# Performance work log

Measured on AMD Instinct MI355X. Metric: run time of the kernel, lower is better.

Reference implementation:

```python
import jax, jax.numpy as jnp
import numpy as np
import math

B, LL, LP = 16, 256, 1024
HID, H = 128, 8
SCALE = math.sqrt(HID)


def setup_inputs() -> dict:
    key = jax.random.key(0)
    ks = jax.random.split(key, 20)
    s = 0.02
    inp = {
        "ligand": jax.random.normal(ks[0], (B, LL, HID), jnp.float32),
        "prot": jax.random.normal(ks[1], (B, LP, HID), jnp.float32),
        "inter": jax.random.uniform(ks[2], (B, 1, LL, LP), jnp.float32),
        # projection weights stored as [in, out] (x @ W + b)
        "Wl1": jax.random.normal(ks[3], (HID, HID * H), jnp.float32) * s,
        "bl1": jnp.zeros((HID * H,), jnp.float32),
        "Wl2": jax.random.normal(ks[4], (HID, HID * H), jnp.float32) * s,
        "bl2": jnp.zeros((HID * H,), jnp.float32),
        "Wp1": jax.random.normal(ks[5], (HID, HID * H), jnp.float32) * s,
        "bp1": jnp.zeros((HID * H,), jnp.float32),
        "Wp2": jax.random.normal(ks[6], (HID, HID * H), jnp.float32) * s,
        "bp2": jnp.zeros((HID * H,), jnp.float32),
        "W11": jax.random.normal(ks[7], (HID * H, HID), jnp.float32) * s,
        "b11": jnp.zeros((HID,), jnp.float32),
        "W12": jax.random.normal(ks[8], (2 * HID, HID), jnp.float32) * s,
        "b12": jnp.zeros((HID,), jnp.float32),
        "W21": jax.random.normal(ks[9], (HID * H, HID), jnp.float32) * s,
        "b21": jnp.zeros((HID,), jnp.float32),
        "W22": jax.random.normal(ks[10], (2 * HID, HID), jnp.float32) * s,
        "b22": jnp.zeros((HID,), jnp.float32),
    }
    return inp


def _heads(x):
    # [B, L, H*D] -> [B, H, L, D]
    b, l, _ = x.shape
    return x.reshape(b, l, H, HID).transpose(0, 2, 1, 3)


def reference(ligand, prot, inter, Wl1, bl1, Wl2, bl2, Wp1, bp1, Wp2, bp2,
              W11, b11, W12, b12, W21, b21, W22, b22):
    relu = jax.nn.relu
    l1 = _heads(relu(ligand @ Wl1 + bl1))   # [B,H,LL,D]
    l2 = _heads(relu(ligand @ Wl2 + bl2))   # [B,H,LL,D]
    p1 = _heads(relu(prot @ Wp1 + bp1))     # [B,H,LP,D]
    p2 = _heads(relu(prot @ Wp2 + bp2))     # [B,H,LP,D]

    energy = jnp.einsum('bhld,bhpd->bhlp', l1, p1) / SCALE
    att = jax.nn.softmax(energy * inter, axis=-1)  # dropout is identity at eval

    # ligand branch: att @ prot2 -> [B,LL,H*D]
    lig3 = jnp.einsum('bhlp,bhpd->blhd', att, p2).reshape(B, LL, H * HID)
    lig3 = jnp.concatenate([lig3 @ W11 + b11, ligand], axis=2)
    lig3 = relu(lig3 @ W12 + b12)

    # protein branch: att^T @ ligand2 -> [B,LP,H*D]
    prot3 = jnp.einsum('bhlp,bhld->bphd', att, l2).reshape(B, LP, H * HID)
    prot3 = jnp.concatenate([prot3 @ W21 + b21, prot], axis=2)
    prot3 = relu(prot3 @ W22 + b22)
    return (lig3, prot3)
```

## Files before the change

kernel.cpp:

```cpp
#include <hip/hip_runtime.h>
#include <hip/hip_bf16.h>

typedef unsigned short u16;
typedef __attribute__((ext_vector_type(4))) float f32x4;
typedef __attribute__((ext_vector_type(4))) unsigned int u32x4;
typedef __attribute__((ext_vector_type(4))) unsigned short u16x4;
typedef __attribute__((ext_vector_type(8))) unsigned short u16x8;
typedef __attribute__((ext_vector_type(8))) __bf16 bf16x8;

__device__ inline float u2f(u16 u) {
    union { unsigned int i; float f; } x; x.i = ((unsigned int)u) << 16; return x.f;
}
__device__ inline u16 f2u(float f) {
    __hip_bfloat16 b = __float2bfloat16(f);
    return *reinterpret_cast<u16*>(&b);
}
__device__ inline f32x4 mfma16(bf16x8 a, bf16x8 b, f32x4 c) {
    return __builtin_amdgcn_mfma_f32_16x16x32_bf16(a, b, c, 0, 0, 0);
}
__device__ inline void gload_lds16(const u16* g, u16* l) {
    __builtin_amdgcn_global_load_lds(
        (const __attribute__((address_space(1))) unsigned int*)g,
        (__attribute__((address_space(3))) unsigned int*)l, 16, 0, 0);
}

__global__ __launch_bounds__(256)
void proj_kernel(const u16* __restrict__ ligb, const u16* __restrict__ protb,
                 const u16* __restrict__ Wl1t, const u16* __restrict__ Wl2t,
                 const u16* __restrict__ Wp1t, const u16* __restrict__ Wp2t,
                 const float* __restrict__ bl1, const float* __restrict__ bl2,
                 const float* __restrict__ bp1, const float* __restrict__ bp2,
                 u16* __restrict__ l1v, u16* __restrict__ l2tv,
                 u16* __restrict__ p1v, u16* __restrict__ p2tv)
{
    __shared__ __align__(16) u16 As[128 * 64];
    __shared__ __align__(16) u16 Bs[128 * 64];
    const int y = blockIdx.y;
    const u16* A; const u16* B; const float* bias; u16* Out;
    int mode, logL, my;
    if (y < 32)       { A = ligb;  B = Wl1t; bias = bl1; Out = l1v;  mode = 1; logL = 8;  my = y; }
    else if (y < 64)  { A = ligb;  B = Wl2t; bias = bl2; Out = l2tv; mode = 3; logL = 8;  my = y - 32; }
    else if (y < 192) { A = protb; B = Wp1t; bias = bp1; Out = p1v;  mode = 1; logL = 10; my = y - 64; }
    else              { A = protb; B = Wp2t; bias = bp2; Out = p2tv; mode = 3; logL = 10; my = y - 192; }
    const int n0 = blockIdx.x * 128, m0 = my * 128;
    const int tid = threadIdx.x;
    const int w = tid >> 6, lane = tid & 63, q = lane >> 4, li = lane & 15;
    const int wr = w >> 1, wc = w & 1;

    const int srow = tid >> 3;
    const int cg = (tid & 7) ^ (srow & 7);
    const int ldsbase = ((tid >> 6) * 8) * 64;

    f32x4 acc[4][4];
    #pragma unroll
    for (int i = 0; i < 4; i++)
        #pragma unroll
        for (int j = 0; j < 4; j++) acc[i][j] = (f32x4){0.f, 0.f, 0.f, 0.f};

    #pragma unroll
    for (int kt = 0; kt < 128; kt += 64) {
        const u16* Ab = A + (long)m0 * 128 + kt + cg * 8;
        const u16* Bb = B + (long)n0 * 128 + kt + cg * 8;
        #pragma unroll
        for (int c = 0; c < 4; c++) {
            gload_lds16(Ab + (long)(c * 32 + srow) * 128, &As[ldsbase + c * 32 * 64]);
            gload_lds16(Bb + (long)(c * 32 + srow) * 128, &Bs[ldsbase + c * 32 * 64]);
        }
        __syncthreads();
        #pragma unroll
        for (int s = 0; s < 2; s++) {
            const int cp = ((s * 4 + q) ^ (li & 7)) * 8;
            bf16x8 av[4], bv[4];
            #pragma unroll
            for (int i = 0; i < 4; i++)
                av[i] = *(bf16x8*)&As[(wr * 64 + i * 16 + li) * 64 + cp];
            #pragma unroll
            for (int j = 0; j < 4; j++)
                bv[j] = *(bf16x8*)&Bs[(wc * 64 + j * 16 + li) * 64 + cp];
            #pragma unroll
            for (int i = 0; i < 4; i++)
                #pragma unroll
                for (int j = 0; j < 4; j++)
                    acc[i][j] = mfma16(av[i], bv[j], acc[i][j]);
        }
        __syncthreads();
    }

    const int Lm = (1 << logL) - 1;
    #pragma unroll
    for (int i = 0; i < 4; i++) {
        #pragma unroll
        for (int j = 0; j < 4; j++) {
            const int col = n0 + wc * 64 + j * 16 + li;
            const float bvs = bias[col];
            if (mode == 3) {
                const int row0 = m0 + wr * 64 + i * 16 + q * 4;
                long base = ((long)(((row0 >> logL) * 8 + (col >> 7)) * 128
                            + (col & 127)) << logL) + (row0 & Lm);
                u16x4 o;
                #pragma unroll
                for (int r = 0; r < 4; r++)
                    o[r] = f2u(fmaxf(acc[i][j][r] + bvs, 0.f));
                *(u16x4*)(Out + base) = o;
            } else {
                #pragma unroll
                for (int r = 0; r < 4; r++) {
                    const int row = m0 + wr * 64 + i * 16 + q * 4 + r;
                    long addr = ((long)((row >> logL) * 8 + (col >> 7)) << (logL + 7))
                              + ((long)(row & Lm) << 7) + (col & 127);
                    Out[addr] = f2u(fmaxf(acc[i][j][r] + bvs, 0.f));
                }
            }
        }
    }
}

__global__ __launch_bounds__(512)
void av_kernel(const u16* __restrict__ att, const u16* __restrict__ p2t,
               const u16* __restrict__ l2t,
               u16* __restrict__ lig3, u16* __restrict__ prot3)
{
    __shared__ __align__(16) u16 As[256 * 64];
    __shared__ __align__(16) u16 Bs[128 * 64];
    __shared__ __align__(16) u16 T[64 * 256];
    const int bid = blockIdx.x;
    const int tid = threadIdx.x;
    const int w = tid >> 6, lane = tid & 63, q = lane >> 4, li = lane & 15;
    const int wr = w >> 1, wc = w & 1;

    f32x4 acc[4][4];
    #pragma unroll
    for (int i = 0; i < 4; i++)
        #pragma unroll
        for (int j = 0; j < 4; j++) acc[i][j] = (f32x4){0.f, 0.f, 0.f, 0.f};

    if (bid < 128) {
        const int bh = bid;
        const u16* A = att + (long)bh * 262144;
        const u16* B = p2t + (long)bh * 131072;
        const int srow = tid >> 3;
        const int cg = (tid & 7) ^ (srow & 7);
        const int ldsbase = ((tid >> 6) * 8) * 64;

        for (int kt = 0; kt < 1024; kt += 64) {
            const u16* Ab = A + kt + cg * 8;
            const u16* Bb = B + kt + cg * 8;
            #pragma unroll
            for (int c = 0; c < 4; c++)
                gload_lds16(Ab + (long)(c * 64 + srow) * 1024,
                            &As[ldsbase + c * 64 * 64]);
            #pragma unroll
            for (int c = 0; c < 2; c++)
                gload_lds16(Bb + (long)(c * 64 + srow) * 1024,
                            &Bs[ldsbase + c * 64 * 64]);
            __syncthreads();
            #pragma unroll
            for (int s = 0; s < 2; s++) {
                const int cp = ((s * 4 + q) ^ (li & 7)) * 8;
                bf16x8 av[4], bv[4];
                #pragma unroll
                for (int i = 0; i < 4; i++)
                    av[i] = *(bf16x8*)&As[(wr * 64 + i * 16 + li) * 64 + cp];
                #pragma unroll
                for (int j = 0; j < 4; j++)
                    bv[j] = *(bf16x8*)&Bs[(wc * 64 + j * 16 + li) * 64 + cp];
                #pragma unroll
                for (int i = 0; i < 4; i++)
                    #pragma unroll
                    for (int j = 0; j < 4; j++)
                        acc[i][j] = mfma16(av[i], bv[j], acc[i][j]);
            }
            __syncthreads();
        }

        const long obase = ((long)(bh >> 3) * 256) * 1024 + (long)(bh & 7) * 128;
        #pragma unroll
        for (int i = 0; i < 4; i++)
            #pragma unroll
            for (int j = 0; j < 4; j++) {
                const int col = wc * 64 + j * 16 + li;
                #pragma unroll
                for (int r = 0; r < 4; r++) {
                    const int row = wr * 64 + i * 16 + q * 4 + r;
                    lig3[obase + (long)row * 1024 + col] = f2u(acc[i][j][r]);
                }
            }
    } else {
        const int pb = bid - 128;
        const int bh = pb >> 2;
        const int m0 = (pb & 3) * 256;
        const u16* A = att + (long)bh * 262144;
        const u16* B = l2t + (long)bh * 32768;
        const int w6 = tid >> 6;
        const int i5 = (tid >> 5) & 1;
        const int srow = tid >> 3;
        const int cg = (tid & 7) ^ (srow & 7);
        const int bldsbase = w6 * 8 * 64;

        for (int kt = 0; kt < 256; kt += 64) {
            #pragma unroll
            for (int c = 0; c < 4; c++) {
                gload_lds16(A + (long)(kt + w6 * 8 + c * 2 + i5) * 1024
                              + m0 + (tid & 31) * 8,
                            &T[w6 * 2048 + c * 512]);
            }
            #pragma unroll
            for (int c = 0; c < 2; c++)
                gload_lds16(B + (long)(c * 64 + srow) * 256 + kt + cg * 8,
                            &Bs[bldsbase + c * 64 * 64]);
            __syncthreads();

            #pragma unroll
            for (int pass = 0; pass < 4; pass++) {
                const int p = pass * 64 + (tid & 63);
                union { u16 e[8]; u32x4 v; } tmp;
                #pragma unroll
                for (int e = 0; e < 8; e++)
                    tmp.e[e] = T[(w6 * 8 + e) * 256 + p];
                *(u32x4*)&As[p * 64 + ((w6 ^ (p & 7)) * 8)] = tmp.v;
            }
            __syncthreads();

            #pragma unroll
            for (int s = 0; s < 2; s++) {
                const int cp = ((s * 4 + q) ^ (li & 7)) * 8;
                bf16x8 av[4], bv[4];
                #pragma unroll
                for (int i = 0; i < 4; i++)
                    av[i] = *(bf16x8*)&As[(wr * 64 + i * 16 + li) * 64 + cp];
                #pragma unroll
                for (int j = 0; j < 4; j++)
                    bv[j] = *(bf16x8*)&Bs[(wc * 64 + j * 16 + li) * 64 + cp];
                #pragma unroll
                for (int i = 0; i < 4; i++)
                    #pragma unroll
                    for (int j = 0; j < 4; j++)
                        acc[i][j] = mfma16(av[i], bv[j], acc[i][j]);
            }
            __syncthreads();
        }

        const long obase = ((long)(bh >> 3) * 1024 + m0) * 1024 + (long)(bh & 7) * 128;
        #pragma unroll
        for (int i = 0; i < 4; i++)
            #pragma unroll
            for (int j = 0; j < 4; j++) {
                const int col = wc * 64 + j * 16 + li;
                #pragma unroll
                for (int r = 0; r < 4; r++) {
                    const int row = wr * 64 + i * 16 + q * 4 + r;
                    prot3[obase + (long)row * 1024 + col] = f2u(acc[i][j][r]);
                }
            }
    }
}

__global__ __launch_bounds__(256)
void finals_kernel(const u16* __restrict__ lig3, const u16* __restrict__ ligb,
                   const u16* __restrict__ WstL, const float* __restrict__ bcL,
                   float* __restrict__ out0,
                   const u16* __restrict__ prot3, const u16* __restrict__ protb,
                   const u16* __restrict__ WstP, const float* __restrict__ bcP,
                   float* __restrict__ out1)
{
    __shared__ __align__(16) u16 As[128 * 64];
    __shared__ __align__(16) u16 Bs[128 * 64];
    const int y = blockIdx.y;
    const u16 *A, *A2, *B; const float* bias; float* Out; int my;
    if (y < 32) { A = lig3;  A2 = ligb;  B = WstL; bias = bcL; Out = out0; my = y; }
    else        { A = prot3; A2 = protb; B = WstP; bias = bcP; Out = out1; my = y - 32; }
    const int m0 = my * 128;
    const int tid = threadIdx.x;
    const int w = tid >> 6, lane = tid & 63, q = lane >> 4, li = lane & 15;
    const int wr = w >> 1, wc = w & 1;

    const int srow = tid >> 3;
    const int cg = (tid & 7) ^ (srow & 7);
    const int ldsbase = ((tid >> 6) * 8) * 64;

    f32x4 acc[4][4];
    #pragma unroll
    for (int i = 0; i < 4; i++)
        #pragma unroll
        for (int j = 0; j < 4; j++) acc[i][j] = (f32x4){0.f, 0.f, 0.f, 0.f};

    for (int kt = 0; kt < 1152; kt += 64) {
        const u16* Abase; long lda; int ktA;
        if (kt >= 1024) { Abase = A2; lda = 128; ktA = kt - 1024; }
        else            { Abase = A;  lda = 1024; ktA = kt; }
        const u16* Ab = Abase + (long)m0 * lda + ktA + cg * 8;
        const u16* Bb = B + kt + cg * 8;
        #pragma unroll
        for (int c = 0; c < 4; c++) {
            gload_lds16(Ab + (long)(c * 32 + srow) * lda,  &As[ldsbase + c * 32 * 64]);
            gload_lds16(Bb + (long)(c * 32 + srow) * 1152, &Bs[ldsbase + c * 32 * 64]);
        }
        __syncthreads();
        #pragma unroll
        for (int s = 0; s < 2; s++) {
            const int cp = ((s * 4 + q) ^ (li & 7)) * 8;
            bf16x8 av[4], bv[4];
            #pragma unroll
            for (int i = 0; i < 4; i++)
                av[i] = *(bf16x8*)&As[(wr * 64 + i * 16 + li) * 64 + cp];
            #pragma unroll
            for (int j = 0; j < 4; j++)
                bv[j] = *(bf16x8*)&Bs[(wc * 64 + j * 16 + li) * 64 + cp];
            #pragma unroll
            for (int i = 0; i < 4; i++)
                #pragma unroll
                for (int j = 0; j < 4; j++)
                    acc[i][j] = mfma16(av[i], bv[j], acc[i][j]);
        }
        __syncthreads();
    }

    #pragma unroll
    for (int i = 0; i < 4; i++)
        #pragma unroll
        for (int j = 0; j < 4; j++) {
            const int col = wc * 64 + j * 16 + li;
            const float bvs = bias[col];
            #pragma unroll
            for (int r = 0; r < 4; r++) {
                const int row = m0 + wr * 64 + i * 16 + q * 4 + r;
                Out[(long)row * 128 + col] = fmaxf(acc[i][j][r] + bvs, 0.f);
            }
        }
}

__global__ __launch_bounds__(512, 4)
void attn_kernel(const u16* __restrict__ l1, const u16* __restrict__ p1,
                 const u16* __restrict__ interb, u16* __restrict__ att)
{
    __shared__ __align__(16) u16 S[32 * 1024];
    const int id = blockIdx.x;
    const int bh = (id & 7) * 16 + (id >> 6);
    const int mt = (id >> 3) & 7;
    const int b  = bh >> 3;
    const int m0 = mt * 32;
    const int tid = threadIdx.x;
    const float rscale = 0.08838834764831845f;

    {
        const int w = tid >> 6, lane = tid & 63, q = lane >> 4, li = lane & 15;
        bf16x8 af[2][4];
        #pragma unroll
        for (int g = 0; g < 2; g++) {
            const u16* lp = l1 + ((long)bh * 256 + m0 + g * 16 + li) * 128 + q * 8;
            #pragma unroll
            for (int s = 0; s < 4; s++) af[g][s] = *(const bf16x8*)(lp + s * 32);
        }
        const u16* bp0 = p1 + ((long)bh * 1024 + w * 128 + li) * 128 + q * 8;
        #pragma unroll
        for (int pf = 0; pf < 8; pf++) {
            const u16* bp = bp0 + (long)pf * 2048;
            bf16x8 bv[4];
            #pragma unroll
            for (int s = 0; s < 4; s++) bv[s] = *(const bf16x8*)(bp + s * 32);
            f32x4 acc0 = (f32x4){0.f, 0.f, 0.f, 0.f};
            f32x4 acc1 = (f32x4){0.f, 0.f, 0.f, 0.f};
            #pragma unroll
            for (int s = 0; s < 4; s++) {
                acc0 = mfma16(af[0][s], bv[s], acc0);
                acc1 = mfma16(af[1][s], bv[s], acc1);
            }
            const int col = w * 128 + pf * 16 + li;
            #pragma unroll
            for (int r = 0; r < 4; r++) {
                const int row0 = q * 4 + r;
                S[(row0 << 10) + (col ^ ((row0 >> 2) << 4))] = f2u(acc0[r] * rscale);
                const int row1 = 16 + q * 4 + r;
                S[(row1 << 10) + (col ^ ((row1 >> 2) << 4))] = f2u(acc1[r] * rscale);
            }
        }
    }
    __syncthreads();

    const int row = tid >> 4;
    const int lj  = tid & 15;
    const int l   = m0 + row;
    const int sw2 = (row >> 2) << 4;
    const u16* ib = interb + ((long)b * 256 + l) * 1024;

    float mx = -1e30f;
    #pragma unroll
    for (int blk = 0; blk < 8; blk++) {
        const int c = blk * 128 + lj * 8;
        u16* sp = &S[(row << 10) + (c ^ sw2)];
        u16x8 s8 = *(u16x8*)sp;
        u16x8 i8 = *(const u16x8*)(ib + c);
        u16x8 o8;
        #pragma unroll
        for (int e = 0; e < 8; e++) {
            float v = u2f(s8[e]) * u2f(i8[e]);
            mx = fmaxf(mx, v);
            o8[e] = f2u(v);
        }
        *(u16x8*)sp = o8;
    }
    #pragma unroll
    for (int d = 1; d < 16; d <<= 1) mx = fmaxf(mx, __shfl_xor(mx, d, 64));

    float z = 0.f;
    #pragma unroll
    for (int blk = 0; blk < 8; blk++) {
        const int c = blk * 128 + lj * 8;
        u16x8 p8 = *(u16x8*)&S[(row << 10) + (c ^ sw2)];
        #pragma unroll
        for (int e = 0; e < 8; e++) z += __expf(u2f(p8[e]) - mx);
    }
    #pragma unroll
    for (int d = 1; d < 16; d <<= 1) z += __shfl_xor(z, d, 64);
    const float inv = 1.f / z;

    u16* op = att + ((long)bh * 256 + l) * 1024;
    #pragma unroll
    for (int blk = 0; blk < 8; blk++) {
        const int c = blk * 128 + lj * 8;
        u16x8 p8 = *(u16x8*)&S[(row << 10) + (c ^ sw2)];
        u16x8 o8;
        #pragma unroll
        for (int e = 0; e < 8; e++)
            o8[e] = f2u(__expf(u2f(p8[e]) - mx) * inv);
        *(u16x8*)(op + c) = o8;
    }
}

struct TPF { const float* src; u16* dst; int R; int C; };
struct TPF8 { TPF t[8]; };

__global__ __launch_bounds__(256)
void cvtw_kernel(TPF8 args)
{
    TPF tp = args.t[blockIdx.z];
    const int c0 = blockIdx.x * 32, r0 = blockIdx.y * 32;
    if (c0 >= tp.C || r0 >= tp.R) return;
    __shared__ u16 tile[32][33];
    const int tx = threadIdx.x & 31, ty = threadIdx.x >> 5;
    #pragma unroll
    for (int i = 0; i < 4; i++)
        tile[ty + i * 8][tx] = f2u(tp.src[(long)(r0 + ty + i * 8) * tp.C + c0 + tx]);
    __syncthreads();
    #pragma unroll
    for (int i = 0; i < 4; i++)
        tp.dst[(long)(c0 + ty + i * 8) * tp.R + r0 + tx] = tile[tx][ty + i * 8];
}

__global__ __launch_bounds__(256)
void wcomb_kernel(const u16* __restrict__ Wm0, const u16* __restrict__ Wo0,
                  const float* __restrict__ bm0, const float* __restrict__ bo0,
                  u16* __restrict__ Wst0, float* __restrict__ bc0,
                  const u16* __restrict__ Wm1, const u16* __restrict__ Wo1,
                  const float* __restrict__ bm1, const float* __restrict__ bo1,
                  u16* __restrict__ Wst1, float* __restrict__ bc1)
{
    const int zz = blockIdx.y;
    const u16* Wm = zz ? Wm1 : Wm0;
    const u16* Wo = zz ? Wo1 : Wo0;
    const float* bmid = zz ? bm1 : bm0;
    const float* bout = zz ? bo1 : bo0;
    u16* Wst = zz ? Wst1 : Wst0;
    float* bc = zz ? bc1 : bc0;
    const int n = blockIdx.x;
    const int tid = threadIdx.x;
    __shared__ float wrow[128];
    if (tid < 128) wrow[tid] = u2f(Wo[n * 256 + tid]);
    __syncthreads();
    for (int k = tid; k < 1024; k += 256) {
        float acc = 0.f;
        #pragma unroll 4
        for (int j = 0; j < 128; j++) acc += wrow[j] * u2f(Wm[(long)j * 1024 + k]);
        Wst[(long)n * 1152 + k] = f2u(acc);
    }
    if (tid < 128) Wst[(long)n * 1152 + 1024 + tid] = Wo[n * 256 + 128 + tid];
    if (tid == 0) {
        float acc = bout[n];
        for (int j = 0; j < 128; j++) acc += bmid[j] * wrow[j];
        bc[n] = acc;
    }
}

__global__ __launch_bounds__(256)
void cvt3_kernel(const float* __restrict__ a, u16* __restrict__ da, int na,
                 const float* __restrict__ b, u16* __restrict__ db, int nb,
                 const float* __restrict__ c, u16* __restrict__ dc, int nc)
{
    const int zz = blockIdx.y;
    const float* s = zz == 0 ? a : (zz == 1 ? b : c);
    u16* d = zz == 0 ? da : (zz == 1 ? db : dc);
    const int n = zz == 0 ? na : (zz == 1 ? nb : nc);
    const int i = (blockIdx.x * 256 + threadIdx.x) * 4;
    if (i >= n) return;
    const float4 v = *(const float4*)(s + i);
    u16x4 o;
    o.x = f2u(v.x); o.y = f2u(v.y); o.z = f2u(v.z); o.w = f2u(v.w);
    *(u16x4*)(d + i) = o;
}

extern "C" void kernel_launch(void* const* d_in, const int* in_sizes, int n_in,
                              void* d_out, int out_size, void* d_ws, size_t ws_size,
                              hipStream_t stream)
{
    (void)in_sizes; (void)n_in; (void)out_size; (void)ws_size;
    const float* ligand = (const float*)d_in[0];
    const float* prot   = (const float*)d_in[1];
    const float* inter  = (const float*)d_in[2];
    const float* Wl1 = (const float*)d_in[3];  const float* bl1 = (const float*)d_in[4];
    const float* Wl2 = (const float*)d_in[5];  const float* bl2 = (const float*)d_in[6];
    const float* Wp1 = (const float*)d_in[7];  const float* bp1 = (const float*)d_in[8];
    const float* Wp2 = (const float*)d_in[9];  const float* bp2 = (const float*)d_in[10];
    const float* W11 = (const float*)d_in[11]; const float* b11 = (const float*)d_in[12];
    const float* W12 = (const float*)d_in[13]; const float* b12 = (const float*)d_in[14];
    const float* W21 = (const float*)d_in[15]; const float* b21 = (const float*)d_in[16];
    const float* W22 = (const float*)d_in[17]; const float* b22 = (const float*)d_in[18];

    float* out0 = (float*)d_out;
    float* out1 = out0 + (size_t)16 * 256 * 128;

    u16* ws = (u16*)d_ws;
    size_t off = 0;
    auto alloc = [&](size_t n) { u16* p = ws + off; off += n; return p; };
    u16* ligb  = alloc(524288);
    u16* protb = alloc(2097152);
    u16* l1v   = alloc(4194304);
    u16* l2t   = alloc(4194304);
    u16* p1v   = alloc(16777216);
    u16* p2t   = alloc(16777216);
    u16* attv  = alloc(33554432);
    u16* lig3  = alloc(4194304);
    u16* prot3 = alloc(16777216);
    u16* Wl1t  = alloc(131072);
    u16* Wl2t  = alloc(131072);
    u16* Wp1t  = alloc(131072);
    u16* Wp2t  = alloc(131072);
    u16* W11t  = alloc(131072);
    u16* W21t  = alloc(131072);
    u16* W12t  = alloc(32768);
    u16* W22t  = alloc(32768);
    u16* WstL  = alloc(147456);
    u16* WstP  = alloc(147456);
    float* bcL = (float*)alloc(256);
    float* bcP = (float*)alloc(256);

    u16* interb = lig3;

    cvt3_kernel<<<dim3(4096, 3), 256, 0, stream>>>(
        ligand, ligb, 524288, prot, protb, 2097152, inter, interb, 4194304);

    TPF8 tp;
    tp.t[0] = {Wl1, Wl1t, 128, 1024};
    tp.t[1] = {Wl2, Wl2t, 128, 1024};
    tp.t[2] = {Wp1, Wp1t, 128, 1024};
    tp.t[3] = {Wp2, Wp2t, 128, 1024};
    tp.t[4] = {W11, W11t, 1024, 128};
    tp.t[5] = {W21, W21t, 1024, 128};
    tp.t[6] = {W12, W12t, 256, 128};
    tp.t[7] = {W22, W22t, 256, 128};
    cvtw_kernel<<<dim3(32, 32, 8), 256, 0, stream>>>(tp);

    wcomb_kernel<<<dim3(128, 2), 256, 0, stream>>>(
        W11t, W12t, b11, b12, WstL, bcL,
        W21t, W22t, b21, b22, WstP, bcP);

    proj_kernel<<<dim3(8, 320), 256, 0, stream>>>(
        ligb, protb, Wl1t, Wl2t, Wp1t, Wp2t,
        bl1, bl2, bp1, bp2, l1v, l2t, p1v, p2t);

    attn_kernel<<<dim3(1024), 512, 0, stream>>>(l1v, p1v, interb, attv);

    av_kernel<<<dim3(640), 512, 0, stream>>>(attv, p2t, l2t, lig3, prot3);

    finals_kernel<<<dim3(1, 160), 256, 0, stream>>>(
        lig3, ligb, WstL, bcL, out0,
        prot3, protb, WstP, bcP, out1);
}
```

Before: 294.1 us.

## Keep attention scores in registers, remap av blocks, halve finals tile rows

The attention kernel now keeps the QK^T scores in MFMA accumulators, multiplies by the interaction map in registers, and does the softmax max and sum reductions with shuffles plus small cross-wave shared arrays. This removes the 64KB shared score buffer, which should raise occupancy. The AV kernel assigns blocks so that the five blocks for one batch-head run next to each other, aiming for L2 reuse of the attention tile. The finals GEMM tiles drop from 128 to 64 rows, doubling the grid for better CU fill. The trade-offs are scattered 2-byte global loads of the interaction map and stores of the attention output in the MFMA layout instead of 16-byte vectors.

Measured after the change: 311.4 us. +5.9%, slower.

```diff
diff --git a/kernel.cpp b/kernel.cpp
--- a/kernel.cpp
+++ b/kernel.cpp
@@ -123,7 +123,10 @@
     __shared__ __align__(16) u16 As[256 * 64];
     __shared__ __align__(16) u16 Bs[128 * 64];
     __shared__ __align__(16) u16 T[64 * 256];
-    const int bid = blockIdx.x;
+    const int id = blockIdx.x;
+    const int slot = id >> 3;
+    const int bh = (id & 7) * 16 + slot / 5;
+    const int role = slot % 5;
     const int tid = threadIdx.x;
     const int w = tid >> 6, lane = tid & 63, q = lane >> 4, li = lane & 15;
     const int wr = w >> 1, wc = w & 1;
@@ -134,8 +137,7 @@
         #pragma unroll
         for (int j = 0; j < 4; j++) acc[i][j] = (f32x4){0.f, 0.f, 0.f, 0.f};
 
-    if (bid < 128) {
-        const int bh = bid;
+    if (role == 0) {
         const u16* A = att + (long)bh * 262144;
         const u16* B = p2t + (long)bh * 131072;
         const int srow = tid >> 3;
@@ -186,9 +188,7 @@
                 }
             }
     } else {
-        const int pb = bid - 128;
-        const int bh = pb >> 2;
-        const int m0 = (pb & 3) * 256;
+        const int m0 = (role - 1) * 256;
         const u16* A = att + (long)bh * 262144;
         const u16* B = l2t + (long)bh * 32768;
         const int w6 = tid >> 6;
@@ -263,13 +263,13 @@
                    const u16* __restrict__ WstP, const float* __restrict__ bcP,
                    float* __restrict__ out1)
 {
-    __shared__ __align__(16) u16 As[128 * 64];
+    __shared__ __align__(16) u16 As[64 * 64];
     __shared__ __align__(16) u16 Bs[128 * 64];
     const int y = blockIdx.y;
     const u16 *A, *A2, *B; const float* bias; float* Out; int my;
-    if (y < 32) { A = lig3;  A2 = ligb;  B = WstL; bias = bcL; Out = out0; my = y; }
-    else        { A = prot3; A2 = protb; B = WstP; bias = bcP; Out = out1; my = y - 32; }
-    const int m0 = my * 128;
+    if (y < 64) { A = lig3;  A2 = ligb;  B = WstL; bias = bcL; Out = out0; my = y; }
+    else        { A = prot3; A2 = protb; B = WstP; bias = bcP; Out = out1; my = y - 64; }
+    const int m0 = my * 64;
     const int tid = threadIdx.x;
     const int w = tid >> 6, lane = tid & 63, q = lane >> 4, li = lane & 15;
     const int wr = w >> 1, wc = w & 1;
@@ -278,9 +278,9 @@
     const int cg = (tid & 7) ^ (srow & 7);
     const int ldsbase = ((tid >> 6) * 8) * 64;
 
-    f32x4 acc[4][4];
-    #pragma unroll
-    for (int i = 0; i < 4; i++)
+    f32x4 acc[2][4];
+    #pragma unroll
+    for (int i = 0; i < 2; i++)
         #pragma unroll
         for (int j = 0; j < 4; j++) acc[i][j] = (f32x4){0.f, 0.f, 0.f, 0.f};
 
@@ -291,23 +291,24 @@
         const u16* Ab = Abase + (long)m0 * lda + ktA + cg * 8;
         const u16* Bb = B + kt + cg * 8;
         #pragma unroll
-        for (int c = 0; c < 4; c++) {
+        for (int c = 0; c < 2; c++)
             gload_lds16(Ab + (long)(c * 32 + srow) * lda,  &As[ldsbase + c * 32 * 64]);
+        #pragma unroll
+        for (int c = 0; c < 4; c++)
             gload_lds16(Bb + (long)(c * 32 + srow) * 1152, &Bs[ldsbase + c * 32 * 64]);
-        }
         __syncthreads();
         #pragma unroll
         for (int s = 0; s < 2; s++) {
             const int cp = ((s * 4 + q) ^ (li & 7)) * 8;
-            bf16x8 av[4], bv[4];
-            #pragma unroll
-            for (int i = 0; i < 4; i++)
-                av[i] = *(bf16x8*)&As[(wr * 64 + i * 16 + li) * 64 + cp];
+            bf16x8 av[2], bv[4];
+            #pragma unroll
+            for (int i = 0; i < 2; i++)
+                av[i] = *(bf16x8*)&As[(wr * 32 + i * 16 + li) * 64 + cp];
             #pragma unroll
             for (int j = 0; j < 4; j++)
                 bv[j] = *(bf16x8*)&Bs[(wc * 64 + j * 16 + li) * 64 + cp];
             #pragma unroll
-            for (int i = 0; i < 4; i++)
+            for (int i = 0; i < 2; i++)
                 #pragma unroll
                 for (int j = 0; j < 4; j++)
                     acc[i][j] = mfma16(av[i], bv[j], acc[i][j]);
@@ -316,115 +317,167 @@
     }
 
     #pragma unroll
-    for (int i = 0; i < 4; i++)
+    for (int i = 0; i < 2; i++)
         #pragma unroll
         for (int j = 0; j < 4; j++) {
             const int col = wc * 64 + j * 16 + li;
             const float bvs = bias[col];
             #pragma unroll
             for (int r = 0; r < 4; r++) {
-                const int row = m0 + wr * 64 + i * 16 + q * 4 + r;
+                const int row = m0 + wr * 32 + i * 16 + q * 4 + r;
                 Out[(long)row * 128 + col] = fmaxf(acc[i][j][r] + bvs, 0.f);
             }
         }
 }
 
-__global__ __launch_bounds__(512, 4)
+__global__ __launch_bounds__(512)
 void attn_kernel(const u16* __restrict__ l1, const u16* __restrict__ p1,
                  const u16* __restrict__ interb, u16* __restrict__ att)
 {
-    __shared__ __align__(16) u16 S[32 * 1024];
+    __shared__ float wred[8][32];
+    __shared__ float wsum[8][32];
     const int id = blockIdx.x;
     const int bh = (id & 7) * 16 + (id >> 6);
     const int mt = (id >> 3) & 7;
     const int b  = bh >> 3;
     const int m0 = mt * 32;
     const int tid = threadIdx.x;
+    const int w = tid >> 6, lane = tid & 63, q = lane >> 4, li = lane & 15;
     const float rscale = 0.08838834764831845f;
 
-    {
-        const int w = tid >> 6, lane = tid & 63, q = lane >> 4, li = lane & 15;
-        bf16x8 af[2][4];
-        #pragma unroll
-        for (int g = 0; g < 2; g++) {
-            const u16* lp = l1 + ((long)bh * 256 + m0 + g * 16 + li) * 128 + q * 8;
-            #pragma unroll
-            for (int s = 0; s < 4; s++) af[g][s] = *(const bf16x8*)(lp + s * 32);
-        }
-        const u16* bp0 = p1 + ((long)bh * 1024 + w * 128 + li) * 128 + q * 8;
+    bf16x8 af[2][4];
+    #pragma unroll
+    for (int g = 0; g < 2; g++) {
+        const u16* lp = l1 + ((long)bh * 256 + m0 + g * 16 + li) * 128 + q * 8;
+        #pragma unroll
+        for (int s = 0; s < 4; s++) af[g][s] = *(const bf16x8*)(lp + s * 32);
+    }
+
+    f32x4 acc[2][8];
+    #pragma unroll
+    for (int g = 0; g < 2; g++)
+        #pragma unroll
+        for (int pf = 0; pf < 8; pf++) acc[g][pf] = (f32x4){0.f, 0.f, 0.f, 0.f};
+
+    const u16* bp0 = p1 + ((long)bh * 1024 + w * 128 + li) * 128 + q * 8;
+    #pragma unroll
+    for (int pf = 0; pf < 8; pf++) {
+        bf16x8 bv[4];
+        #pragma unroll
+        for (int s = 0; s < 4; s++)
+            bv[s] = *(const bf16x8*)(bp0 + (long)pf * 2048 + s * 32);
+        #pragma unroll
+        for (int s = 0; s < 4; s++) {
+            acc[0][pf] = mfma16(af[0][s], bv[s], acc[0][pf]);
+            acc[1][pf] = mfma16(af[1][s], bv[s], acc[1][pf]);
+        }
+    }
+
+    const u16* ib = interb + ((long)b * 256 + m0) * 1024;
+    float rmax[2][4];
+    #pragma unroll
+    for (int g = 0; g < 2; g++)
+        #pragma unroll
+        for (int r = 0; r < 4; r++) rmax[g][r] = -1e30f;
+    #pragma unroll
+    for (int g = 0; g < 2; g++)
         #pragma unroll
         for (int pf = 0; pf < 8; pf++) {
-            const u16* bp = bp0 + (long)pf * 2048;
-            bf16x8 bv[4];
-            #pragma unroll
-            for (int s = 0; s < 4; s++) bv[s] = *(const bf16x8*)(bp + s * 32);
-            f32x4 acc0 = (f32x4){0.f, 0.f, 0.f, 0.f};
-            f32x4 acc1 = (f32x4){0.f, 0.f, 0.f, 0.f};
-            #pragma unroll
-            for (int s = 0; s < 4; s++) {
-                acc0 = mfma16(af[0][s], bv[s], acc0);
-                acc1 = mfma16(af[1][s], bv[s], acc1);
-            }
             const int col = w * 128 + pf * 16 + li;
             #pragma unroll
             for (int r = 0; r < 4; r++) {
-                const int row0 = q * 4 + r;
-                S[(row0 << 10) + (col ^ ((row0 >> 2) << 4))] = f2u(acc0[r] * rscale);
-                const int row1 = 16 + q * 4 + r;
-                S[(row1 << 10) + (col ^ ((row1 >> 2) << 4))] = f2u(acc1[r] * rscale);
-            }
-        }
+                const float iv = u2f(ib[(g * 16 + q * 4 + r) * 1024 + col]);
+                const float v = acc[g][pf][r] * rscale * iv;
+                acc[g][pf][r] = v;
+                rmax[g][r] = fmaxf(rmax[g][r], v);
+            }
+        }
+    #pragma unroll
+    for (int g = 0; g < 2; g++)
+        #pragma unroll
+        for (int r = 0; r < 4; r++) {
+            float m = rmax[g][r];
+            #pragma unroll
+            for (int d = 1; d < 16; d <<= 1) m = fmaxf(m, __shfl_xor(m, d, 64));
+            rmax[g][r] = m;
+        }
+    if (li == 0) {
+        #pragma unroll
+        for (int g = 0; g < 2; g++)
+            #pragma unroll
+            for (int r = 0; r < 4; r++)
+                wred[w][g * 16 + q * 4 + r] = rmax[g][r];
     }
     __syncthreads();
 
-    const int row = tid >> 4;
-    const int lj  = tid & 15;
-    const int l   = m0 + row;
-    const int sw2 = (row >> 2) << 4;
-    const u16* ib = interb + ((long)b * 256 + l) * 1024;
-
-    float mx = -1e30f;
-    #pragma unroll
-    for (int blk = 0; blk < 8; blk++) {
-        const int c = blk * 128 + lj * 8;
-        u16* sp = &S[(row << 10) + (c ^ sw2)];
-        u16x8 s8 = *(u16x8*)sp;
-        u16x8 i8 = *(const u16x8*)(ib + c);
-        u16x8 o8;
-        #pragma unroll
-        for (int e = 0; e < 8; e++) {
-            float v = u2f(s8[e]) * u2f(i8[e]);
-            mx = fmaxf(mx, v);
-            o8[e] = f2u(v);
-        }
-        *(u16x8*)sp = o8;
-    }
-    #pragma unroll
-    for (int d = 1; d < 16; d <<= 1) mx = fmaxf(mx, __shfl_xor(mx, d, 64));
-
-    float z = 0.f;
-    #pragma unroll
-    for (int blk = 0; blk < 8; blk++) {
-        const int c = blk * 128 + lj * 8;
-        u16x8 p8 = *(u16x8*)&S[(row << 10) + (c ^ sw2)];
-        #pragma unroll
-        for (int e = 0; e < 8; e++) z += __expf(u2f(p8[e]) - mx);
-    }
-    #pragma unroll
-    for (int d = 1; d < 16; d <<= 1) z += __shfl_xor(z, d, 64);
-    const float inv = 1.f / z;
-
-    u16* op = att + ((long)bh * 256 + l) * 1024;
-    #pragma unroll
-    for (int blk = 0; blk < 8; blk++) {
-        const int c = blk * 128 + lj * 8;
-        u16x8 p8 = *(u16x8*)&S[(row << 10) + (c ^ sw2)];
-        u16x8 o8;
-        #pragma unroll
-        for (int e = 0; e < 8; e++)
-            o8[e] = f2u(__expf(u2f(p8[e]) - mx) * inv);
-        *(u16x8*)(op + c) = o8;
-    }
+    float gmax[2][4];
+    #pragma unroll
+    for (int g = 0; g < 2; g++)
+        #pragma unroll
+        for (int r = 0; r < 4; r++) {
+            const int row = g * 16 + q * 4 + r;
+            float m = wred[0][row];
+            #pragma unroll
+            for (int wv = 1; wv < 8; wv++) m = fmaxf(m, wred[wv][row]);
+            gmax[g][r] = m;
+        }
+
+    float zs[2][4];
+    #pragma unroll
+    for (int g = 0; g < 2; g++)
+        #pragma unroll
+        for (int r = 0; r < 4; r++) zs[g][r] = 0.f;
+    #pragma unroll
+    for (int g = 0; g < 2; g++)
+        #pragma unroll
+        for (int pf = 0; pf < 8; pf++)
+            #pragma unroll
+            for (int r = 0; r < 4; r++) {
+                const float e = __expf(acc[g][pf][r] - gmax[g][r]);
+                acc[g][pf][r] = e;
+                zs[g][r] += e;
+            }
+    #pragma unroll
+    for (int g = 0; g < 2; g++)
+        #pragma unroll
+        for (int r = 0; r < 4; r++) {
+            float z = zs[g][r];
+            #pragma unroll
+            for (int d = 1; d < 16; d <<= 1) z += __shfl_xor(z, d, 64);
+            zs[g][r] = z;
+        }
+    if (li == 0) {
+        #pragma unroll
+        for (int g = 0; g < 2; g++)
+            #pragma unroll
+            for (int r = 0; r < 4; r++)
+                wsum[w][g * 16 + q * 4 + r] = zs[g][r];
+    }
+    __syncthreads();
+
+    float inv[2][4];
+    #pragma unroll
+    for (int g = 0; g < 2; g++)
+        #pragma unroll
+        for (int r = 0; r < 4; r++) {
+            const int row = g * 16 + q * 4 + r;
+            float z = wsum[0][row];
+            #pragma unroll
+            for (int wv = 1; wv < 8; wv++) z += wsum[wv][row];
+            inv[g][r] = 1.f / z;
+        }
+
+    u16* ob = att + ((long)bh * 256 + m0) * 1024;
+    #pragma unroll
+    for (int g = 0; g < 2; g++)
+        #pragma unroll
+        for (int pf = 0; pf < 8; pf++) {
+            const int col = w * 128 + pf * 16 + li;
+            #pragma unroll
+            for (int r = 0; r < 4; r++)
+                ob[(g * 16 + q * 4 + r) * 1024 + col] =
+                    f2u(acc[g][pf][r] * inv[g][r]);
+        }
 }
 
 struct TPF { const float* src; u16* dst; int R; int C; };
@@ -571,7 +624,7 @@
 
     av_kernel<<<dim3(640), 512, 0, stream>>>(attv, p2t, l2t, lig3, prot3);
 
-    finals_kernel<<<dim3(1, 160), 256, 0, stream>>>(
+    finals_kernel<<<dim3(1, 320), 256, 0, stream>>>(
         lig3, ligb, WstL, bcL, out0,
         prot3, protb, WstP, bcP, out1);
 }
```
